# Kernel optimization log

Measured on AMD Instinct MI355X. Metric: run time of the kernel, lower is better.

The kernel has to match this reference:

```python
import jax, jax.numpy as jnp
import numpy as np

NUM_CLASSES = 2
THRESHOLD = 0.35
NEGPOS_RATIO = 3
VAR0, VAR1 = 0.1, 0.2
ALPHA = 1.0
B, P, G = 16, 131072, 64


def _iou(a, b):
    # a: [G,4] point-form gts, b: [P,4] point-form priors -> [G,P]
    tl = jnp.maximum(a[:, None, :2], b[None, :, :2])
    br = jnp.minimum(a[:, None, 2:], b[None, :, 2:])
    wh = jnp.clip(br - tl, 0.0)
    inter = wh[..., 0] * wh[..., 1]
    area_a = (a[:, 2] - a[:, 0]) * (a[:, 3] - a[:, 1])
    area_b = (b[:, 2] - b[:, 0]) * (b[:, 3] - b[:, 1])
    return inter / (area_a[:, None] + area_b[None, :] - inter)


def setup_inputs() -> dict:
    key = jax.random.key(0)
    k1, k2, k3, k4, k5, k6 = jax.random.split(key, 6)
    loc_preds = jax.random.normal(k1, (B, P, 4), jnp.float32)
    cls_preds = jax.random.normal(k2, (B, P, NUM_CLASSES), jnp.float32)
    # priors in center form [cx, cy, w, h]
    pcxy = jax.random.uniform(k3, (P, 2), jnp.float32)
    pwh = 0.02 + 0.15 * jax.random.uniform(k4, (P, 2), jnp.float32)
    priorbox = jnp.concatenate([pcxy, pwh], axis=1)
    # ground-truth boxes; stored as [y1,x1,y2,x2,label] so that the module's
    # column permutation [1,0,3,2] yields valid point-form [x1,y1,x2,y2]
    xy1 = 0.8 * jax.random.uniform(k5, (B, G, 2), jnp.float32)
    wh = 0.02 + 0.1 * jax.random.uniform(k6, (B, G, 2), jnp.float32)
    xy2 = xy1 + wh
    boxes_perm = jnp.stack([xy1[..., 1], xy1[..., 0], xy2[..., 1], xy2[..., 0]], axis=-1)
    labels = jnp.ones((B, G, 1), jnp.float32)  # single foreground class (face)
    targets = jnp.concatenate([boxes_perm, labels], axis=-1)
    return {"loc_preds": loc_preds, "cls_preds": cls_preds,
            "priorbox": priorbox, "targets": targets}


def _loss(loc_preds, cls_preds, priorbox, targets):
    priors_c = priorbox[: loc_preds.shape[1], :]
    priors_pt = jnp.concatenate(
        [priors_c[:, :2] - priors_c[:, 2:] / 2,
         priors_c[:, :2] + priors_c[:, 2:] / 2], axis=1)
    num_g = targets.shape[1]

    def match_one(t):
        gts = t[:, :4][:, jnp.array([1, 0, 3, 2])]  # -> point form [x1,y1,x2,y2]
        labels = t[:, 4]
        ov = _iou(gts, priors_pt)                    # [G,P]
        best_prior_idx = jnp.argmax(ov, axis=1)      # [G]
        bto = jnp.max(ov, axis=0)                    # [P] best gt overlap per prior
        bti = jnp.argmax(ov, axis=0)                 # [P]
        bto = bto.at[best_prior_idx].set(2.0)        # force best prior per gt
        bti = bti.at[best_prior_idx].set(jnp.arange(num_g))
        conf = jnp.where(bto < THRESHOLD, 0.0, labels[bti])
        m = gts[bti]                                 # [P,4] matched gt boxes
        g_cxcy = ((m[:, :2] + m[:, 2:]) / 2 - priors_c[:, :2]) / (VAR0 * priors_c[:, 2:])
        g_wh = jnp.log((m[:, 2:] - m[:, :2]) / priors_c[:, 2:]) / VAR1
        return conf, jnp.concatenate([g_cxcy, g_wh], axis=1)

    cls_batch, loc_batch = jax.vmap(match_one)(targets)
    cls_batch = jax.lax.stop_gradient(cls_batch)   # targets require no grad
    loc_batch = jax.lax.stop_gradient(loc_batch)

    pos = cls_batch > 0                              # [B,P]
    npos = jnp.sum(pos)

    # smooth-L1 over positive priors, mean over selected elements (size_average)
    d = loc_preds - loc_batch
    ad = jnp.abs(d)
    sl1 = jnp.where(ad < 1.0, 0.5 * d * d, ad - 0.5)
    loss_loc = jnp.sum(sl1 * pos[..., None]) / jnp.maximum(npos * 4, 1).astype(sl1.dtype)

    # per-prior CE loss for hard-negative mining
    ignore = cls_batch < 0
    lbl = jnp.where(ignore, 0.0, cls_batch).astype(jnp.int32)
    lse = jax.nn.logsumexp(cls_preds, axis=-1)       # [B,P]
    gathered = jnp.take_along_axis(cls_preds, lbl[..., None], axis=-1)[..., 0]
    loss_c = jnp.where(pos | ignore, 0.0, lse - gathered)
    # two-stage sort: rank of each prior by descending loss
    loss_idx = jnp.argsort(-loss_c, axis=1)
    idx_rank = jnp.argsort(loss_idx, axis=1)
    num_pos_img = jnp.sum(pos, axis=1, keepdims=True)
    num_neg = jnp.minimum(NEGPOS_RATIO * num_pos_img, pos.shape[1] - 1)
    neg = idx_rank < num_neg
    mask = pos | neg
    # cross-entropy over mined samples, mean over selected (size_average)
    loss_cls = jnp.sum((lse - gathered) * mask) / jnp.maximum(jnp.sum(mask), 1).astype(lse.dtype)

    loss = (loss_cls + ALPHA * loss_loc) / npos.astype(lse.dtype)
    return loss, loss_loc, loss_cls


def reference(loc_preds, cls_preds, priorbox, targets):
    return _loss(loc_preds, cls_preds, priorbox, targets)
```

## Files before the change

### kernel.cpp

```cpp
#include <hip/hip_runtime.h>

#define BB 16
#define PP 131072
#define GG 64
#define THRESH 0.35f
#define RMAX 0.086f
#define NCH 32
#define CPR 4096
#define NCC 16
#define CPC 8192

#define OFF_BESTG   0
#define OFF_H1TOT   8192
#define OFF_H1STOT  270336
#define OFF_NPOSI   532480
#define OFF_PCI     532544
#define OFF_LOCI    532608
#define OFF_CIDX    532672
#define OFF_DONE    532736
#define OFF_SELI    532800
#define OFF_RESN    533056
#define OFF_RESK    533120
#define OFF_RESC    533184
#define OFF_RESL    533248
#define OFF_PU8     533312
#define OFF_KEYS    2630464
#define OFF_CAND    11019072

__global__ __launch_bounds__(1024) void k_init(
    unsigned* __restrict__ bestg32, int* __restrict__ nposi, float* __restrict__ pci,
    float* __restrict__ loci, unsigned* __restrict__ cidx, unsigned* __restrict__ done)
{
    const int t = threadIdx.x;
    bestg32[t] = 0u; bestg32[t + 1024] = 0u;
    if (t < BB) { nposi[t] = 0; pci[t] = 0.f; loci[t] = 0.f; cidx[t] = 0u; }
    if (t == BB) *done = 0u;
}

__global__ __launch_bounds__(1024, 8) void k_match(
    const float* __restrict__ priorbox, const float* __restrict__ targets,
    unsigned long long* __restrict__ bestg, unsigned char* __restrict__ pu8,
    unsigned* __restrict__ h1tot, float* __restrict__ h1stot)
{
    __shared__ unsigned msk[8192];
    __shared__ float4 gxy[GG];
    __shared__ unsigned long long sbest[GG];
    const int b = blockIdx.y, chunk = blockIdx.x, tid = threadIdx.x;

    {
        const int zb = (b * NCH + chunk) * 128;
        if (tid < 128) h1tot[zb + tid] = 0u;
        else if (tid < 256) h1stot[zb + tid - 128] = 0.f;
    }
    for (int i = tid; i < 8192; i += 1024) msk[i] = 0u;
    if (tid < GG) {
        const float* t = targets + (size_t)(b * GG + tid) * 5;
        gxy[tid] = make_float4(t[1], t[0], t[3], t[2]);
        sbest[tid] = 0ull;
    }
    __syncthreads();

    {
        const int g = tid & 63, strip = tid >> 6;
        float4 a = gxy[g];
        int cx0 = max(0, (int)((a.x - RMAX) * 64.f));
        int cx1 = min(63, (int)ceilf((a.z + RMAX) * 64.f) - 1);
        int cy0 = max(0, (int)((a.y - RMAX) * 64.f));
        int cy1 = min(63, (int)ceilf((a.w + RMAX) * 64.f) - 1);
        unsigned bit = 1u << (g & 31);
        const int word = (g >> 5);
        for (int cy = cy0 + strip; cy <= cy1; cy += 16)
            for (int cx = cx0; cx <= cx1; cx++)
                atomicOr(&msk[2 * (cy * 64 + cx) + word], bit);
    }
    __syncthreads();

#pragma unroll
    for (int j = 0; j < 4; j++) {
        const int p = chunk * CPR + j * 1024 + tid;
        float4 pr = *reinterpret_cast<const float4*>(priorbox + (size_t)p * 4);
        float hx = 0.5f * pr.z, hy = 0.5f * pr.w;
        float px1 = pr.x - hx, py1 = pr.y - hy;
        float px2 = pr.x + hx, py2 = pr.y + hy;
        float par = (px2 - px1) * (py2 - py1);
        int cx = min(63, max(0, (int)(pr.x * 64.f)));
        int cy = min(63, max(0, (int)(pr.y * 64.f)));
        uint2 mm = *reinterpret_cast<uint2*>(&msk[2 * (cy * 64 + cx)]);
        unsigned long long m = ((unsigned long long)mm.y << 32) | mm.x;
        const unsigned long long notp = (unsigned long long)(~(unsigned)p);
        float bv = -1.f; int bg = 0;
        while (m) {
            const int g0 = __ffsll(m) - 1; m &= m - 1;
            const bool has1 = (m != 0ull);
            const int g1 = has1 ? (__ffsll(m) - 1) : g0;
            if (has1) m &= m - 1;
            float4 a0 = gxy[g0];
            float4 a1 = gxy[g1];
            float w0 = fmaxf(fminf(a0.z, px2) - fmaxf(a0.x, px1), 0.f);
            float h0 = fmaxf(fminf(a0.w, py2) - fmaxf(a0.y, py1), 0.f);
            float w1 = fmaxf(fminf(a1.z, px2) - fmaxf(a1.x, px1), 0.f);
            float h1 = fmaxf(fminf(a1.w, py2) - fmaxf(a1.y, py1), 0.f);
            float ar0 = (a0.z - a0.x) * (a0.w - a0.y);
            float ar1 = (a1.z - a1.x) * (a1.w - a1.y);
            float i0 = w0 * h0, i1 = w1 * h1;
            float v0 = i0 * __builtin_amdgcn_rcpf(ar0 + par - i0);
            float v1 = i1 * __builtin_amdgcn_rcpf(ar1 + par - i1);
            if (v0 > bv) { bv = v0; bg = g0; }
            if (has1 && v1 > bv) { bv = v1; bg = g1; }
            if (v0 > 0.f)
                atomicMax(&sbest[g0],
                          (((unsigned long long)__float_as_uint(v0)) << 32) | notp);
            if (has1 && v1 > 0.f)
                atomicMax(&sbest[g1],
                          (((unsigned long long)__float_as_uint(v1)) << 32) | notp);
        }
        pu8[(size_t)b * PP + p] = (unsigned char)(bg | ((bv >= THRESH) ? 0x80 : 0));
    }

    __syncthreads();
    if (tid < GG) {
        unsigned long long s = sbest[tid];
        if (s) atomicMax(&bestg[b * GG + tid], s);
    }
}

__global__ __launch_bounds__(1024, 8) void k_loss(
    const float* __restrict__ loc_preds, const float* __restrict__ cls_preds,
    const float* __restrict__ priorbox, const float* __restrict__ targets,
    const unsigned long long* __restrict__ bestg, const unsigned char* __restrict__ pu8,
    unsigned* __restrict__ keys, unsigned* __restrict__ h1tot, float* __restrict__ h1stot,
    int* __restrict__ nposi, float* __restrict__ pci, float* __restrict__ loci)
{
    __shared__ unsigned hcnt[4096];
    __shared__ float hsum[4096];
    __shared__ float4 gxy[GG];
    __shared__ float glab[GG];
    __shared__ unsigned blist[GG];
    __shared__ int nb;
    __shared__ float sred[32];
    __shared__ int sredi[16];
    const int b = blockIdx.y, chunk = blockIdx.x, tid = threadIdx.x;
    const int lane = tid & 63, wid = tid >> 6;

    for (int i = tid; i < 4096; i += 1024) { hcnt[i] = 0u; hsum[i] = 0.f; }
    if (tid < GG) {
        const float* t = targets + (size_t)(b * GG + tid) * 5;
        gxy[tid] = make_float4(t[1], t[0], t[3], t[2]);
        glab[tid] = t[4];
    }
    __syncthreads();
    if (tid == 0) {
        int n = 0;
        for (int g = 0; g < GG; g++) {
            unsigned long long m = bestg[b * GG + g];
            if (m) {
                unsigned p = ~((unsigned)(m & 0xFFFFFFFFull));
                if ((int)(p >> 12) == chunk)
                    blist[n++] = (((p & (CPR - 1)) << 6) | (unsigned)g);
            }
        }
        nb = n;
    }
    __syncthreads();

    const int nbl = nb;
    float locpart = 0.f, clspart = 0.f; int cnt = 0;
#pragma unroll
    for (int j = 0; j < 4; j++) {
        const int plocal = j * 1024 + tid;
        const size_t ip = (size_t)b * PP + chunk * CPR + plocal;
        const unsigned m8 = pu8[ip];
        int g = m8 & 63;
        bool pos = (m8 >> 7) != 0;
        for (int i = 0; i < nbl; i++) {
            unsigned e = blist[i];
            if ((int)(e >> 6) == plocal) { pos = true; g = (int)(e & 63u); }
        }
        const float2 cl = *reinterpret_cast<const float2*>(cls_preds + ip * 2);
        const float mx = fmaxf(cl.x, cl.y);
        const float lse = mx + log1pf(expf(fminf(cl.x, cl.y) - mx));
        unsigned key = 0u;
        if (pos && glab[g] > 0.f) {
            float gathered = (((int)glab[g]) == 0) ? cl.x : cl.y;
            clspart += lse - gathered;
            cnt++;
            const int p = chunk * CPR + plocal;
            float4 pr = *reinterpret_cast<const float4*>(priorbox + (size_t)p * 4);
            float4 gt = gxy[g];
            float gcx = ((gt.x + gt.z) * 0.5f - pr.x) / (0.1f * pr.z);
            float gcy = ((gt.y + gt.w) * 0.5f - pr.y) / (0.1f * pr.w);
            float gw = logf((gt.z - gt.x) / pr.z) / 0.2f;
            float gh = logf((gt.w - gt.y) / pr.w) / 0.2f;
            float4 lp = *reinterpret_cast<const float4*>(loc_preds + ip * 4);
            float d0 = lp.x - gcx, d1 = lp.y - gcy, d2 = lp.z - gw, d3 = lp.w - gh;
            float a0 = fabsf(d0), a1 = fabsf(d1), a2 = fabsf(d2), a3 = fabsf(d3);
            locpart += ((a0 < 1.f) ? 0.5f * d0 * d0 : a0 - 0.5f)
                     + ((a1 < 1.f) ? 0.5f * d1 * d1 : a1 - 0.5f)
                     + ((a2 < 1.f) ? 0.5f * d2 * d2 : a2 - 0.5f)
                     + ((a3 < 1.f) ? 0.5f * d3 * d3 : a3 - 0.5f);
        } else {
            float lc = lse - cl.x;
            key = __float_as_uint(lc);
            atomicAdd(&hcnt[key >> 20], 1u);
            atomicAdd(&hsum[key >> 20], lc);
        }
        keys[ip] = key;
    }

    for (int o = 32; o; o >>= 1) {
        locpart += __shfl_xor(locpart, o);
        clspart += __shfl_xor(clspart, o);
        cnt     += __shfl_xor(cnt, o);
    }
    if (lane == 0) { sred[wid] = locpart; sred[16 + wid] = clspart; sredi[wid] = cnt; }
    __syncthreads();
    if (tid == 0) {
        float l = 0.f, c = 0.f; int n = 0;
        for (int i = 0; i < 16; i++) { l += sred[i]; c += sred[16 + i]; n += sredi[i]; }
        if (n)        atomicAdd(&nposi[b], n);
        if (c != 0.f) atomicAdd(&pci[b], c);
        if (l != 0.f) atomicAdd(&loci[b], l);
    }
    __syncthreads();
    for (int i = tid; i < 4096; i += 1024) {
        unsigned cc = hcnt[i];
        if (cc) {
            atomicAdd(&h1tot[b * 4096 + i], cc);
            atomicAdd(&h1stot[b * 4096 + i], hsum[i]);
        }
    }
}

template <int NBINS>
__device__ void find_kth_par(const unsigned* __restrict__ h, int k, int* sel, int* krem)
{
    constexpr int PER = NBINS / 1024;
    __shared__ unsigned wsum_[16];
    __shared__ int res_[2];
    const int tid = threadIdx.x, lane = tid & 63, wid = tid >> 6;
    __syncthreads();
    unsigned own[PER];
    unsigned s = 0;
#pragma unroll
    for (int i = 0; i < PER; i++) { own[i] = h[NBINS - 1 - (tid * PER + i)]; s += own[i]; }
    unsigned incl = s;
    for (int d = 1; d < 64; d <<= 1) {
        unsigned t = __shfl_up(incl, d);
        if (lane >= d) incl += t;
    }
    if (lane == 63) wsum_[wid] = incl;
    if (tid == 0) { res_[0] = -1; res_[1] = 0; }
    __syncthreads();
    unsigned woff = 0;
    for (int w = 0; w < 16; w++) woff += (w < wid) ? wsum_[w] : 0u;
    const unsigned texcl = woff + incl - s;
    if (k > 0 && texcl < (unsigned)k && texcl + s >= (unsigned)k) {
        unsigned run = texcl;
#pragma unroll
        for (int i = 0; i < PER; i++) {
            run += own[i];
            if (run >= (unsigned)k) {
                res_[0] = NBINS - 1 - (tid * PER + i);
                res_[1] = k - (int)(run - own[i]);
                break;
            }
        }
    }
    __syncthreads();
    *sel = res_[0]; *krem = res_[1];
}

__device__ float block_sum_f(float v)
{
    __shared__ float rs[16];
    const int tid = threadIdx.x;
    __syncthreads();
    for (int o = 32; o; o >>= 1) v += __shfl_xor(v, o);
    if ((tid & 63) == 0) rs[tid >> 6] = v;
    __syncthreads();
    float s = 0.f;
    for (int i = 0; i < 16; i++) s += rs[i];
    return s;
}

__global__ __launch_bounds__(1024) void k_compact(
    const unsigned* __restrict__ keys, const unsigned* __restrict__ h1tot,
    const int* __restrict__ nposi, unsigned* __restrict__ cand,
    unsigned* __restrict__ cidx, int* __restrict__ seli)
{
    __shared__ unsigned wcnt[16], wbase[16];
    __shared__ unsigned bbase;
    const int b = blockIdx.y, chunk = blockIdx.x, tid = threadIdx.x;
    const int lane = tid & 63, wid = tid >> 6;

    unsigned kv[8];
#pragma unroll
    for (int j = 0; j < 8; j++)
        kv[j] = keys[(size_t)b * PP + chunk * CPC + j * 1024 + tid];

    const int np = nposi[b];
    const int k = min(3 * np, PP - 1);
    int sel1, kk1;
    find_kth_par<4096>(h1tot + b * 4096, k, &sel1, &kk1);
    if (chunk == 0 && tid == 0) {
        seli[b * 4 + 0] = sel1; seli[b * 4 + 1] = kk1;
        seli[b * 4 + 2] = np;   seli[b * 4 + 3] = k;
    }
    const unsigned s1 = (unsigned)sel1;

    unsigned long long mv[8];
    unsigned wn = 0;
#pragma unroll
    for (int j = 0; j < 8; j++) {
        mv[j] = __ballot((kv[j] >> 20) == s1);
        wn += (unsigned)__popcll(mv[j]);
    }
    if (lane == 0) wcnt[wid] = wn;
    __syncthreads();
    if (tid == 0) {
        unsigned run = 0;
        for (int w = 0; w < 16; w++) { wbase[w] = run; run += wcnt[w]; }
        bbase = run ? atomicAdd(&cidx[b], run) : 0u;
    }
    __syncthreads();
    unsigned run = bbase + wbase[wid];
    const unsigned long long lanemask = (1ull << lane) - 1ull;
#pragma unroll
    for (int j = 0; j < 8; j++) {
        if ((kv[j] >> 20) == s1)
            cand[(size_t)b * PP + run + (unsigned)__popcll(mv[j] & lanemask)] = kv[j];
        run += (unsigned)__popcll(mv[j]);
    }
}

__global__ __launch_bounds__(1024) void k_select(
    const unsigned* __restrict__ cand, const unsigned* __restrict__ cidx,
    const float* __restrict__ h1stot, const int* __restrict__ seli,
    const float* __restrict__ pci, const float* __restrict__ loci,
    int* __restrict__ resn, int* __restrict__ resk,
    float* __restrict__ resc, float* __restrict__ resl,
    unsigned* __restrict__ done, float* __restrict__ out)
{
    __shared__ unsigned ch[1024];
    __shared__ float cs[1024];
    __shared__ int lastflag;
    const int b = blockIdx.x, tid = threadIdx.x;
    const int sel1 = seli[b * 4 + 0], kk1 = seli[b * 4 + 1];
    const int np   = seli[b * 4 + 2], k   = seli[b * 4 + 3];
    const unsigned ncand = cidx[b];

    float nh = 0.f;
    for (int i = tid; i < 4096; i += 1024)
        if (i > sel1) nh += h1stot[b * 4096 + i];
    float negsum_high = block_sum_f(nh);

    __syncthreads();
    ch[tid] = 0u; cs[tid] = 0.f;
    __syncthreads();
    for (unsigned i = tid; i < ncand; i += 1024) {
        unsigned v = cand[(size_t)b * PP + i];
        unsigned bin = (v >> 10) & 1023u;
        atomicAdd(&ch[bin], 1u);
        atomicAdd(&cs[bin], __uint_as_float(v));
    }
    __syncthreads();
    int sel2, kk2;
    find_kth_par<1024>(ch, (sel1 < 0) ? 0 : kk1, &sel2, &kk2);
    float sumhi2 = block_sum_f((sel2 >= 0 && tid > sel2) ? cs[tid] : 0.f);

    __syncthreads();
    ch[tid] = 0u; cs[tid] = 0.f;
    __syncthreads();
    if (sel2 >= 0) {
        for (unsigned i = tid; i < ncand; i += 1024) {
            unsigned v = cand[(size_t)b * PP + i];
            if (((v >> 10) & 1023u) == (unsigned)sel2) {
                atomicAdd(&ch[v & 1023u], 1u);
                atomicAdd(&cs[v & 1023u], __uint_as_float(v));
            }
        }
    }
    __syncthreads();
    int sel3, needeq;
    find_kth_par<1024>(ch, (sel2 < 0) ? 0 : kk2, &sel3, &needeq);
    float sumhi3 = block_sum_f((sel3 >= 0 && tid > sel3) ? cs[tid] : 0.f);

    if (tid == 0) {
        float add = 0.f;
        if (sel3 >= 0 && needeq > 0) {
            unsigned Kstar = ((unsigned)sel1 << 20) | ((unsigned)sel2 << 10) | (unsigned)sel3;
            add = needeq * __uint_as_float(Kstar);
        }
        resn[b] = np;
        resk[b] = k;
        resc[b] = pci[b] + negsum_high + sumhi2 + sumhi3 + add;
        resl[b] = loci[b];
        __threadfence();
        unsigned old = atomicAdd(done, 1u);
        lastflag = (old == BB - 1) ? 1 : 0;
    }
    __syncthreads();
    if (!lastflag || tid != 0) return;

    __threadfence();
    volatile int* vrn = (volatile int*)resn;
    volatile int* vrk = (volatile int*)resk;
    volatile float* vrc = (volatile float*)resc;
    volatile float* vrl = (volatile float*)resl;
    int npt = 0; long long maskc = 0; float clsnum = 0.f, locnum = 0.f;
    for (int b2 = 0; b2 < BB; b2++) {
        npt += vrn[b2];
        maskc += (long long)vrn[b2] + vrk[b2];
        clsnum += vrc[b2];
        locnum += vrl[b2];
    }
    float denom_loc = (float)((4 * npt > 1) ? 4 * npt : 1);
    float denom_cls = (float)((maskc > 1) ? maskc : 1);
    float loss_loc = locnum / denom_loc;
    float loss_cls = clsnum / denom_cls;
    out[0] = (loss_cls + loss_loc) / (float)npt;
    out[1] = loss_loc;
    out[2] = loss_cls;
}

extern "C" void kernel_launch(void* const* d_in, const int* in_sizes, int n_in,
                              void* d_out, int out_size, void* d_ws, size_t ws_size,
                              hipStream_t stream)
{
    const float* loc_preds = (const float*)d_in[0];
    const float* cls_preds = (const float*)d_in[1];
    const float* priorbox  = (const float*)d_in[2];
    const float* targets   = (const float*)d_in[3];
    float* out = (float*)d_out;

    char* ws = (char*)d_ws;
    unsigned long long* bestg = (unsigned long long*)(ws + OFF_BESTG);
    unsigned* h1tot  = (unsigned*)(ws + OFF_H1TOT);
    float*    h1stot = (float*)(ws + OFF_H1STOT);
    int*      nposi  = (int*)(ws + OFF_NPOSI);
    float*    pci    = (float*)(ws + OFF_PCI);
    float*    loci   = (float*)(ws + OFF_LOCI);
    unsigned* cidx   = (unsigned*)(ws + OFF_CIDX);
    unsigned* done   = (unsigned*)(ws + OFF_DONE);
    int*      seli   = (int*)(ws + OFF_SELI);
    int*      resn   = (int*)(ws + OFF_RESN);
    int*      resk   = (int*)(ws + OFF_RESK);
    float*    resc   = (float*)(ws + OFF_RESC);
    float*    resl   = (float*)(ws + OFF_RESL);
    unsigned char* pu8 = (unsigned char*)(ws + OFF_PU8);
    unsigned* keys   = (unsigned*)(ws + OFF_KEYS);
    unsigned* cand   = (unsigned*)(ws + OFF_CAND);

    k_init<<<1, 1024, 0, stream>>>((unsigned*)bestg, nposi, pci, loci, cidx, done);
    k_match<<<dim3(NCH, BB), 1024, 0, stream>>>(priorbox, targets, bestg, pu8,
                                                h1tot, h1stot);
    k_loss<<<dim3(NCH, BB), 1024, 0, stream>>>(loc_preds, cls_preds, priorbox, targets,
                                               bestg, pu8, keys, h1tot, h1stot,
                                               nposi, pci, loci);
    k_compact<<<dim3(NCC, BB), 1024, 0, stream>>>(keys, h1tot, nposi, cand, cidx, seli);
    k_select<<<BB, 1024, 0, stream>>>(cand, cidx, h1stot, seli, pci, loci,
                                      resn, resk, resc, resl, done, out);
}
```

Measured before the change: 99.14 us.

## Drop init and select kernels; use per-chunk partials and last-block-done tail

Removes the init kernel by writing per-chunk partial bestg, npos, cls and loc values that later kernels reduce, instead of global atomics into zeroed buffers. The per-bin float sum histogram is dropped; the high-negatives sum is instead computed directly from the keys held in the compaction kernel. The select stage is merged into the compaction kernel, where the last-arriving block per image runs it. This cuts two launches and the float atomics, at the cost of an extra in-block max reduction over 32 partials and a serialized tail block per image.

```diff
diff --git a/kernel.cpp b/kernel.cpp
--- a/kernel.cpp
+++ b/kernel.cpp
@@ -7,51 +7,37 @@
 #define RMAX 0.086f
 #define NCH 32
 #define CPR 4096
-#define NCC 16
-#define CPC 8192
-
-#define OFF_BESTG   0
-#define OFF_H1TOT   8192
-#define OFF_H1STOT  270336
-#define OFF_NPOSI   532480
-#define OFF_PCI     532544
-#define OFF_LOCI    532608
-#define OFF_CIDX    532672
-#define OFF_DONE    532736
-#define OFF_SELI    532800
-#define OFF_RESN    533056
-#define OFF_RESK    533120
-#define OFF_RESC    533184
-#define OFF_RESL    533248
-#define OFF_PU8     533312
-#define OFF_KEYS    2630464
-#define OFF_CAND    11019072
-
-__global__ __launch_bounds__(1024) void k_init(
-    unsigned* __restrict__ bestg32, int* __restrict__ nposi, float* __restrict__ pci,
-    float* __restrict__ loci, unsigned* __restrict__ cidx, unsigned* __restrict__ done)
-{
-    const int t = threadIdx.x;
-    bestg32[t] = 0u; bestg32[t + 1024] = 0u;
-    if (t < BB) { nposi[t] = 0; pci[t] = 0.f; loci[t] = 0.f; cidx[t] = 0u; }
-    if (t == BB) *done = 0u;
-}
+#define NCT 16
+#define CPT 8192
+
+#define OFF_BESTP   0
+#define OFF_H1TOT   262144
+#define OFF_NPOSP   524288
+#define OFF_PCP     526336
+#define OFF_LOCP    528384
+#define OFF_CIDX    530432
+#define OFF_NEGS    530496
+#define OFF_ARR     530560
+#define OFF_DONE    530624
+#define OFF_RESN    530688
+#define OFF_RESK    530752
+#define OFF_RESC    530816
+#define OFF_RESL    530880
+#define OFF_PU8     530944
+#define OFF_KEYS    2628096
+#define OFF_CAND    11016704
 
 __global__ __launch_bounds__(1024, 8) void k_match(
     const float* __restrict__ priorbox, const float* __restrict__ targets,
-    unsigned long long* __restrict__ bestg, unsigned char* __restrict__ pu8,
-    unsigned* __restrict__ h1tot, float* __restrict__ h1stot)
+    unsigned long long* __restrict__ bestp, unsigned char* __restrict__ pu8,
+    unsigned* __restrict__ h1tot)
 {
     __shared__ unsigned msk[8192];
     __shared__ float4 gxy[GG];
     __shared__ unsigned long long sbest[GG];
     const int b = blockIdx.y, chunk = blockIdx.x, tid = threadIdx.x;
 
-    {
-        const int zb = (b * NCH + chunk) * 128;
-        if (tid < 128) h1tot[zb + tid] = 0u;
-        else if (tid < 256) h1stot[zb + tid - 128] = 0.f;
-    }
+    if (tid < 128) h1tot[b * 4096 + chunk * 128 + tid] = 0u;
     for (int i = tid; i < 8192; i += 1024) msk[i] = 0u;
     if (tid < GG) {
         const float* t = targets + (size_t)(b * GG + tid) * 5;
@@ -118,21 +104,20 @@
     }
 
     __syncthreads();
-    if (tid < GG) {
-        unsigned long long s = sbest[tid];
-        if (s) atomicMax(&bestg[b * GG + tid], s);
-    }
+    if (tid < GG) bestp[(b * NCH + chunk) * GG + tid] = sbest[tid];
 }
 
 __global__ __launch_bounds__(1024, 8) void k_loss(
     const float* __restrict__ loc_preds, const float* __restrict__ cls_preds,
     const float* __restrict__ priorbox, const float* __restrict__ targets,
-    const unsigned long long* __restrict__ bestg, const unsigned char* __restrict__ pu8,
-    unsigned* __restrict__ keys, unsigned* __restrict__ h1tot, float* __restrict__ h1stot,
-    int* __restrict__ nposi, float* __restrict__ pci, float* __restrict__ loci)
-{
+    const unsigned long long* __restrict__ bestp, const unsigned char* __restrict__ pu8,
+    unsigned* __restrict__ keys, unsigned* __restrict__ h1tot,
+    int* __restrict__ nposp, float* __restrict__ pcp, float* __restrict__ locp,
+    unsigned* __restrict__ cidx, float* __restrict__ negs,
+    unsigned* __restrict__ arr, unsigned* __restrict__ done)
+{
+    __shared__ unsigned long long tmp64[2048];
     __shared__ unsigned hcnt[4096];
-    __shared__ float hsum[4096];
     __shared__ float4 gxy[GG];
     __shared__ float glab[GG];
     __shared__ unsigned blist[GG];
@@ -142,17 +127,32 @@
     const int b = blockIdx.y, chunk = blockIdx.x, tid = threadIdx.x;
     const int lane = tid & 63, wid = tid >> 6;
 
-    for (int i = tid; i < 4096; i += 1024) { hcnt[i] = 0u; hsum[i] = 0.f; }
+    if (tid == 0 && chunk == 0) {
+        cidx[b] = 0u; negs[b] = 0.f; arr[b] = 0u;
+        if (b == 0) *done = 0u;
+    }
+
+    tmp64[tid]        = bestp[(b * NCH + (tid >> 6)) * GG + (tid & 63)];
+    tmp64[tid + 1024] = bestp[(b * NCH + 16 + (tid >> 6)) * GG + (tid & 63)];
+    for (int i = tid; i < 4096; i += 1024) hcnt[i] = 0u;
     if (tid < GG) {
         const float* t = targets + (size_t)(b * GG + tid) * 5;
         gxy[tid] = make_float4(t[1], t[0], t[3], t[2]);
         glab[tid] = t[4];
     }
     __syncthreads();
+    for (int s = 16; s > 0; s >>= 1) {
+        if (tid < s * 64) {
+            const int c = tid >> 6, g = tid & 63;
+            unsigned long long a = tmp64[c * 64 + g], d = tmp64[(c + s) * 64 + g];
+            tmp64[c * 64 + g] = d > a ? d : a;
+        }
+        __syncthreads();
+    }
     if (tid == 0) {
         int n = 0;
         for (int g = 0; g < GG; g++) {
-            unsigned long long m = bestg[b * GG + g];
+            unsigned long long m = tmp64[g];
             if (m) {
                 unsigned p = ~((unsigned)(m & 0xFFFFFFFFull));
                 if ((int)(p >> 12) == chunk)
@@ -202,7 +202,6 @@
             float lc = lse - cl.x;
             key = __float_as_uint(lc);
             atomicAdd(&hcnt[key >> 20], 1u);
-            atomicAdd(&hsum[key >> 20], lc);
         }
         keys[ip] = key;
     }
@@ -217,17 +216,14 @@
     if (tid == 0) {
         float l = 0.f, c = 0.f; int n = 0;
         for (int i = 0; i < 16; i++) { l += sred[i]; c += sred[16 + i]; n += sredi[i]; }
-        if (n)        atomicAdd(&nposi[b], n);
-        if (c != 0.f) atomicAdd(&pci[b], c);
-        if (l != 0.f) atomicAdd(&loci[b], l);
+        nposp[b * NCH + chunk] = n;
+        pcp[b * NCH + chunk] = c;
+        locp[b * NCH + chunk] = l;
     }
     __syncthreads();
     for (int i = tid; i < 4096; i += 1024) {
         unsigned cc = hcnt[i];
-        if (cc) {
-            atomicAdd(&h1tot[b * 4096 + i], cc);
-            atomicAdd(&h1stot[b * 4096 + i], hsum[i]);
-        }
+        if (cc) atomicAdd(&h1tot[b * 4096 + i], cc);
     }
 }
 
@@ -283,30 +279,47 @@
     return s;
 }
 
-__global__ __launch_bounds__(1024) void k_compact(
+__global__ __launch_bounds__(1024) void k_tail(
     const unsigned* __restrict__ keys, const unsigned* __restrict__ h1tot,
-    const int* __restrict__ nposi, unsigned* __restrict__ cand,
-    unsigned* __restrict__ cidx, int* __restrict__ seli)
+    const int* __restrict__ nposp, const float* __restrict__ pcp,
+    const float* __restrict__ locp, unsigned* __restrict__ cand,
+    unsigned* __restrict__ cidx, float* __restrict__ negs,
+    unsigned* __restrict__ arr, unsigned* __restrict__ done,
+    int* __restrict__ resn, int* __restrict__ resk,
+    float* __restrict__ resc, float* __restrict__ resl, float* __restrict__ out)
 {
     __shared__ unsigned wcnt[16], wbase[16];
     __shared__ unsigned bbase;
+    __shared__ int snp, lastflag;
+    __shared__ unsigned ch[1024];
+    __shared__ float cs[1024];
     const int b = blockIdx.y, chunk = blockIdx.x, tid = threadIdx.x;
     const int lane = tid & 63, wid = tid >> 6;
 
+    if (tid == 0) {
+        int np = 0;
+        for (int c = 0; c < NCH; c++) np += nposp[b * NCH + c];
+        snp = np;
+    }
     unsigned kv[8];
 #pragma unroll
     for (int j = 0; j < 8; j++)
-        kv[j] = keys[(size_t)b * PP + chunk * CPC + j * 1024 + tid];
-
-    const int np = nposi[b];
+        kv[j] = keys[(size_t)b * PP + chunk * CPT + j * 1024 + tid];
+    __syncthreads();
+    const int np = snp;
     const int k = min(3 * np, PP - 1);
     int sel1, kk1;
     find_kth_par<4096>(h1tot + b * 4096, k, &sel1, &kk1);
-    if (chunk == 0 && tid == 0) {
-        seli[b * 4 + 0] = sel1; seli[b * 4 + 1] = kk1;
-        seli[b * 4 + 2] = np;   seli[b * 4 + 3] = k;
-    }
     const unsigned s1 = (unsigned)sel1;
+
+    float nv = 0.f;
+    if (sel1 >= 0) {
+#pragma unroll
+        for (int j = 0; j < 8; j++)
+            if ((kv[j] >> 20) > s1) nv += __uint_as_float(kv[j]);
+    }
+    float nsum = block_sum_f(nv);
+    if (tid == 0 && nsum != 0.f) atomicAdd(&negs[b], nsum);
 
     unsigned long long mv[8];
     unsigned wn = 0;
@@ -323,38 +336,28 @@
         bbase = run ? atomicAdd(&cidx[b], run) : 0u;
     }
     __syncthreads();
-    unsigned run = bbase + wbase[wid];
-    const unsigned long long lanemask = (1ull << lane) - 1ull;
-#pragma unroll
-    for (int j = 0; j < 8; j++) {
-        if ((kv[j] >> 20) == s1)
-            cand[(size_t)b * PP + run + (unsigned)__popcll(mv[j] & lanemask)] = kv[j];
-        run += (unsigned)__popcll(mv[j]);
-    }
-}
-
-__global__ __launch_bounds__(1024) void k_select(
-    const unsigned* __restrict__ cand, const unsigned* __restrict__ cidx,
-    const float* __restrict__ h1stot, const int* __restrict__ seli,
-    const float* __restrict__ pci, const float* __restrict__ loci,
-    int* __restrict__ resn, int* __restrict__ resk,
-    float* __restrict__ resc, float* __restrict__ resl,
-    unsigned* __restrict__ done, float* __restrict__ out)
-{
-    __shared__ unsigned ch[1024];
-    __shared__ float cs[1024];
-    __shared__ int lastflag;
-    const int b = blockIdx.x, tid = threadIdx.x;
-    const int sel1 = seli[b * 4 + 0], kk1 = seli[b * 4 + 1];
-    const int np   = seli[b * 4 + 2], k   = seli[b * 4 + 3];
+    {
+        unsigned run = bbase + wbase[wid];
+        const unsigned long long lanemask = (1ull << lane) - 1ull;
+#pragma unroll
+        for (int j = 0; j < 8; j++) {
+            if ((kv[j] >> 20) == s1)
+                cand[(size_t)b * PP + run + (unsigned)__popcll(mv[j] & lanemask)] = kv[j];
+            run += (unsigned)__popcll(mv[j]);
+        }
+    }
+
+    __syncthreads();
+    if (tid == 0) {
+        __threadfence();
+        unsigned old = atomicAdd(&arr[b], 1u);
+        lastflag = (old == NCT - 1) ? 1 : 0;
+    }
+    __syncthreads();
+    if (!lastflag) return;
+    __threadfence();
+
     const unsigned ncand = cidx[b];
-
-    float nh = 0.f;
-    for (int i = tid; i < 4096; i += 1024)
-        if (i > sel1) nh += h1stot[b * 4096 + i];
-    float negsum_high = block_sum_f(nh);
-
-    __syncthreads();
     ch[tid] = 0u; cs[tid] = 0.f;
     __syncthreads();
     for (unsigned i = tid; i < ncand; i += 1024) {
@@ -386,6 +389,11 @@
     float sumhi3 = block_sum_f((sel3 >= 0 && tid > sel3) ? cs[tid] : 0.f);
 
     if (tid == 0) {
+        float pcsum = 0.f, locsum = 0.f;
+        for (int c = 0; c < NCH; c++) {
+            pcsum += pcp[b * NCH + c];
+            locsum += locp[b * NCH + c];
+        }
         float add = 0.f;
         if (sel3 >= 0 && needeq > 0) {
             unsigned Kstar = ((unsigned)sel1 << 20) | ((unsigned)sel2 << 10) | (unsigned)sel3;
@@ -393,8 +401,8 @@
         }
         resn[b] = np;
         resk[b] = k;
-        resc[b] = pci[b] + negsum_high + sumhi2 + sumhi3 + add;
-        resl[b] = loci[b];
+        resc[b] = pcsum + negs[b] + sumhi2 + sumhi3 + add;
+        resl[b] = locsum;
         __threadfence();
         unsigned old = atomicAdd(done, 1u);
         lastflag = (old == BB - 1) ? 1 : 0;
@@ -434,30 +442,28 @@
     float* out = (float*)d_out;
 
     char* ws = (char*)d_ws;
-    unsigned long long* bestg = (unsigned long long*)(ws + OFF_BESTG);
-    unsigned* h1tot  = (unsigned*)(ws + OFF_H1TOT);
-    float*    h1stot = (float*)(ws + OFF_H1STOT);
-    int*      nposi  = (int*)(ws + OFF_NPOSI);
-    float*    pci    = (float*)(ws + OFF_PCI);
-    float*    loci   = (float*)(ws + OFF_LOCI);
-    unsigned* cidx   = (unsigned*)(ws + OFF_CIDX);
-    unsigned* done   = (unsigned*)(ws + OFF_DONE);
-    int*      seli   = (int*)(ws + OFF_SELI);
-    int*      resn   = (int*)(ws + OFF_RESN);
-    int*      resk   = (int*)(ws + OFF_RESK);
-    float*    resc   = (float*)(ws + OFF_RESC);
-    float*    resl   = (float*)(ws + OFF_RESL);
+    unsigned long long* bestp = (unsigned long long*)(ws + OFF_BESTP);
+    unsigned* h1tot = (unsigned*)(ws + OFF_H1TOT);
+    int*      nposp = (int*)(ws + OFF_NPOSP);
+    float*    pcp   = (float*)(ws + OFF_PCP);
+    float*    locp  = (float*)(ws + OFF_LOCP);
+    unsigned* cidx  = (unsigned*)(ws + OFF_CIDX);
+    float*    negs  = (float*)(ws + OFF_NEGS);
+    unsigned* arr   = (unsigned*)(ws + OFF_ARR);
+    unsigned* done  = (unsigned*)(ws + OFF_DONE);
+    int*      resn  = (int*)(ws + OFF_RESN);
+    int*      resk  = (int*)(ws + OFF_RESK);
+    float*    resc  = (float*)(ws + OFF_RESC);
+    float*    resl  = (float*)(ws + OFF_RESL);
     unsigned char* pu8 = (unsigned char*)(ws + OFF_PU8);
-    unsigned* keys   = (unsigned*)(ws + OFF_KEYS);
-    unsigned* cand   = (unsigned*)(ws + OFF_CAND);
-
-    k_init<<<1, 1024, 0, stream>>>((unsigned*)bestg, nposi, pci, loci, cidx, done);
-    k_match<<<dim3(NCH, BB), 1024, 0, stream>>>(priorbox, targets, bestg, pu8,
-                                                h1tot, h1stot);
+    unsigned* keys  = (unsigned*)(ws + OFF_KEYS);
+    unsigned* cand  = (unsigned*)(ws + OFF_CAND);
+
+    k_match<<<dim3(NCH, BB), 1024, 0, stream>>>(priorbox, targets, bestp, pu8, h1tot);
     k_loss<<<dim3(NCH, BB), 1024, 0, stream>>>(loc_preds, cls_preds, priorbox, targets,
-                                               bestg, pu8, keys, h1tot, h1stot,
-                                               nposi, pci, loci);
-    k_compact<<<dim3(NCC, BB), 1024, 0, stream>>>(keys, h1tot, nposi, cand, cidx, seli);
-    k_select<<<BB, 1024, 0, stream>>>(cand, cidx, h1stot, seli, pci, loci,
-                                      resn, resk, resc, resl, done, out);
-}
+                                               bestp, pu8, keys, h1tot,
+                                               nposp, pcp, locp, cidx, negs, arr, done);
+    k_tail<<<dim3(NCT, BB), 1024, 0, stream>>>(keys, h1tot, nposp, pcp, locp, cand,
+                                               cidx, negs, arr, done,
+                                               resn, resk, resc, resl, out);
+}
```

Measured after the change: 111.8 us. 12.7% more time.
